# Kernel tuning notes

Hardware: AMD Instinct MI355X
Metric: run time of the kernel (lower is better)

The kernel has to match this reference:

```python
import jax, jax.numpy as jnp
import numpy as np

BS, N, IN_DIM, OUT_DIM = 16, 2048, 32, 64
CHEB_K, E_NODE, T_D = 3, 10, 8
EMBED = E_NODE + T_D  # 18, matches weights_pool dim 0
TOPK = 10


def setup_inputs() -> dict:
    key = jax.random.key(0)
    ks = jax.random.split(key, 7)
    return {
        "x": jax.random.normal(ks[0], (BS, N, IN_DIM), jnp.float32),
        "node_emb": jax.random.normal(ks[1], (N, E_NODE), jnp.float32),
        "t": jax.random.normal(ks[2], (BS, T_D), jnp.float32),
        "n_t": jax.random.normal(ks[3], (BS, T_D), jnp.float32),
        "p": jax.random.normal(ks[4], (BS, 1, 1), jnp.float32),
        "weights_pool": jax.random.normal(ks[5], (EMBED, CHEB_K, IN_DIM, OUT_DIM), jnp.float32) * 0.1,
        "bias_pool": jax.random.normal(ks[6], (EMBED, OUT_DIM), jnp.float32) * 0.1,
    }


def reference(x, node_emb, t, n_t, p, weights_pool, bias_pool):
    bs, n, _ = x.shape
    # static adjacency from node embeddings, broadcast over batch: [bs, N, N]
    a = (node_emb @ node_emb.T)[None, :, :]
    # temporal scalar correction: bmm([bs,1,td],[bs,td,1]) -> [bs,1,1]
    a_t = jnp.einsum('bd,bd->b', n_t, t)[:, None, None]
    _a = a + a_t
    # period branch: scaled relu adjacency, then dynamic topK sparsify
    pre = jax.nn.relu((1.0 + 0.3 * jax.nn.sigmoid(p)) * _a)  # [bs, N, N]
    # topK tie-break noise (torch.rand_like * 0.01); deterministic key here
    noise = jax.random.uniform(jax.random.key(42), pre.shape, jnp.float32) * 0.01
    _, idx = jax.lax.top_k(pre + noise, TOPK)  # idx: [bs, N, TOPK]
    mask = jnp.zeros_like(pre).at[
        jnp.arange(bs)[:, None, None], jnp.arange(n)[None, :, None], idx
    ].set(1.0)
    # masked entries stay 0 (not -inf) before softmax, as in the original
    A = jax.nn.softmax(pre * mask, axis=2)
    # Chebyshev polynomial supports: T0=I, T1=A, Tk = 2*A@T(k-1) - T(k-2)
    I = jnp.broadcast_to(jnp.eye(n, dtype=x.dtype), (bs, n, n))
    supports = [I, A]
    for _ in range(2, CHEB_K):
        supports.append(2.0 * (A @ supports[-1]) - supports[-2])
    S = jnp.stack(supports, axis=1)  # [bs, K, N, N]
    # node-adaptive embedding: cat(node_emb, n_t) -> [bs, N, EMBED]
    ne = jnp.concatenate(
        [jnp.broadcast_to(node_emb[None], (bs, n, E_NODE)),
         jnp.broadcast_to(n_t[:, None, :], (bs, n, T_D))], axis=-1)
    # graph conv features: [bs, N, K, in]
    x_g = jnp.einsum('bknm,bmc->bnkc', S, x)
    bias = ne @ bias_pool  # [bs, N, out]
    # fused per-node dynamic-weight contraction:
    # original: W = einsum(bnd,dkio->bnkio); out = einsum(bnki,bnkio->bno)
    out = jnp.einsum('bnki,bnd,dkio->bno', x_g, ne, weights_pool) + bias
    return out
```

## Files before the change

### kernel.cpp

```cpp
#include <hip/hip_runtime.h>
#include <hip/hip_bf16.h>


constexpr int BS = 16, NN_ = 2048, CIN = 32, OUT = 64, TK = 10;
constexpr int ROWS = BS * NN_;

__device__ __forceinline__ void tf2x32(unsigned x0, unsigned x1,
                                       unsigned& o0, unsigned& o1) {
  const unsigned k0 = 0u, k1 = 42u;
  const unsigned ks2 = k0 ^ k1 ^ 0x1BD11BDAu;
#define TF_R(rot) { x0 += x1; x1 = (x1 << rot) | (x1 >> (32 - rot)); x1 ^= x0; }
  x0 += k0; x1 += k1;
  TF_R(13) TF_R(15) TF_R(26) TF_R(6)
  x0 += k1; x1 += ks2 + 1u;
  TF_R(17) TF_R(29) TF_R(16) TF_R(24)
  x0 += ks2; x1 += k0 + 2u;
  TF_R(13) TF_R(15) TF_R(26) TF_R(6)
  x0 += k0; x1 += k1 + 3u;
  TF_R(17) TF_R(29) TF_R(16) TF_R(24)
  x0 += k1; x1 += ks2 + 4u;
  TF_R(13) TF_R(15) TF_R(26) TF_R(6)
  x0 += ks2; x1 += k0 + 5u;
#undef TF_R
  o0 = x0; o1 = x1;
}

__device__ __forceinline__ float noise_val(unsigned flat) {
  unsigned o0, o1; tf2x32(0u, flat, o0, o1);
  unsigned bits = o0 ^ o1;
  float u = __uint_as_float((bits >> 9) | 0x3f800000u) - 1.0f;
  return 0.01f * u;
}

__global__ __launch_bounds__(256) void k_a0(const float* __restrict__ ne,
                                            float* __restrict__ A0) {
  int gid = blockIdx.x * 256 + threadIdx.x;
  int n = gid >> 11, m = gid & 2047;
  float acc = 0.f;
  #pragma unroll
  for (int d = 0; d < 10; ++d) acc = fmaf(ne[n * 10 + d], ne[m * 10 + d], acc);
  A0[gid] = acc;
}

__global__ __launch_bounds__(256) void k_topk(const float* __restrict__ A0,
                                              const float* __restrict__ t,
                                              const float* __restrict__ n_t,
                                              const float* __restrict__ p,
                                              float* __restrict__ cinv,
                                              int* __restrict__ idxb,
                                              float* __restrict__ wgt) {
  const int n0 = blockIdx.x * 2;
  const int warp = threadIdx.x >> 6, lane = threadIdx.x & 63;
  const int ln = warp >> 1;
  const int n = n0 + ln;
  const int bh = (warp & 1) * 8;

  __shared__ float rowS[2][2048];
  __shared__ float candA[4][128];
  __shared__ int   candM[4][128];
  __shared__ unsigned long long keyS[4][128];

  {
    const float4* src = (const float4*)(A0 + (size_t)n0 * 2048);
    float4* dst = (float4*)rowS;
    for (int i = threadIdx.x; i < 1024; i += 256) dst[i] = src[i];
  }
  __syncthreads();

  float a[32];
  #pragma unroll
  for (int j = 0; j < 8; ++j) {
    float4 f = ((const float4*)rowS[ln])[j * 64 + lane];
    a[j * 4 + 0] = f.x; a[j * 4 + 1] = f.y;
    a[j * 4 + 2] = f.z; a[j * 4 + 3] = f.w;
  }

  float lm = -3.4e38f;
  #pragma unroll
  for (int j = 0; j < 32; ++j) lm = fmaxf(lm, a[j]);

  float last = 3.4e38f;
  for (int rd = 0; rd < 11; ++rd) {
    float x = (lm < last) ? lm : -3.4e38f;
    #pragma unroll
    for (int off = 32; off > 0; off >>= 1) x = fmaxf(x, __shfl_xor(x, off));
    last = x;
  }
  const float T = last - 0.0101f;

  int cnt = 0;
  #pragma unroll
  for (int slot = 0; slot < 32; ++slot) {
    bool c = (a[slot] >= T);
    unsigned long long mk = __ballot(c);
    if (c) {
      int pos = cnt + __popcll(mk & ((1ull << lane) - 1ull));
      if (pos < 128) {
        candA[warp][pos] = a[slot];
        candM[warp][pos] = ((slot >> 2) << 8) + (lane << 2) + (slot & 3);
      }
    }
    cnt += (int)__popcll(mk);
  }
  const int C = cnt < 128 ? cnt : 128;
  const bool two = (C > 64);

  __syncthreads();

  float a0c = 0.f, a1c = 0.f; int m0 = 0, m1 = 0;
  if (lane < C) { a0c = candA[warp][lane]; m0 = candM[warp][lane]; }
  if (two && lane + 64 < C) { a1c = candA[warp][lane + 64]; m1 = candM[warp][lane + 64]; }

  for (int bi = 0; bi < 8; ++bi) {
    const int b = bh + bi;
    const int r = (b << 11) | n;

    float at = 0.f;
    #pragma unroll
    for (int d = 0; d < 8; ++d) at = fmaf(n_t[b * 8 + d], t[b * 8 + d], at);
    const float s = 1.0f + 0.3f * (1.0f / (1.0f + expf(-p[b])));

    float pre0 = fmaxf(s * (a0c + at), 0.f);
    unsigned long long k0 = 0ull;
    if (lane < C) {
      float key0 = pre0 + noise_val((unsigned)r * 2048u + (unsigned)m0);
      k0 = ((unsigned long long)__float_as_uint(key0) << 32) |
           (unsigned)(2047 - m0);
      keyS[warp][lane] = k0;
    }
    float pre1 = 0.f;
    unsigned long long k1 = 0ull;
    if (two) {
      if (lane + 64 < C) {
        pre1 = fmaxf(s * (a1c + at), 0.f);
        float key1 = pre1 + noise_val((unsigned)r * 2048u + (unsigned)m1);
        k1 = ((unsigned long long)__float_as_uint(key1) << 32) |
             (unsigned)(2047 - m1);
      }
      keyS[warp][lane + 64] = k1;
    }
    __syncthreads();

    int rank0 = 0, rank1 = 0;
    for (int j2 = 0; j2 < C; ++j2) {
      unsigned long long kj = keyS[warp][j2];
      rank0 += (kj > k0) ? 1 : 0;
      if (two) rank1 += (kj > k1) ? 1 : 0;
    }
    bool w0 = (lane < C) && (rank0 < 10);
    bool w1 = two && (lane + 64 < C) && (rank1 < 10);

    float e0 = w0 ? expf(pre0) : 0.f;
    float e1 = w1 ? expf(pre1) : 0.f;
    float sum = e0 + e1;
    #pragma unroll
    for (int off = 32; off > 0; off >>= 1) sum += __shfl_xor(sum, off);
    const float ci = 1.0f / (2038.0f + sum);

    unsigned long long mk0 = __ballot(w0);
    if (w0) {
      int pos = __popcll(mk0 & ((1ull << lane) - 1ull));
      idxb[r * 10 + pos] = m0;
      wgt[r * 10 + pos] = (e0 - 1.0f) * ci;
    }
    if (two) {
      unsigned long long mk1 = __ballot(w1);
      int base = __popcll(mk0);
      if (w1) {
        int pos = base + __popcll(mk1 & ((1ull << lane) - 1ull));
        idxb[r * 10 + pos] = m1;
        wgt[r * 10 + pos] = (e1 - 1.0f) * ci;
      }
    }
    if (lane == 0) cinv[r] = ci;
    __syncthreads();
  }
}

__global__ __launch_bounds__(256) void k_colsum_p(const float* __restrict__ in,
                                                  double* __restrict__ part) {
  const int b = blockIdx.x >> 4, ch = blockIdx.x & 15;
  const int c = threadIdx.x & 31, g = threadIdx.x >> 5;
  double acc = 0.0;
  for (int m = ch * 128 + g; m < ch * 128 + 128; m += 8)
    acc += (double)in[(((b << 11) + m) << 5) + c];
  __shared__ double red[8][32];
  red[g][c] = acc;
  __syncthreads();
  if (g == 0) {
    double s2 = red[0][c];
    #pragma unroll
    for (int i = 1; i < 8; ++i) s2 += red[i][c];
    part[(((b << 4) + ch) << 5) + c] = s2;
  }
}

__global__ __launch_bounds__(512) void k_colsum_f(const double* __restrict__ part,
                                                  float* __restrict__ cs) {
  const int b = threadIdx.x >> 5, c = threadIdx.x & 31;
  double s2 = 0.0;
  #pragma unroll
  for (int ch = 0; ch < 16; ++ch) s2 += part[(((b << 4) + ch) << 5) + c];
  cs[(b << 5) + c] = (float)s2;
}

__global__ __launch_bounds__(256) void k_axpy(const float* __restrict__ x,
                                              const float* __restrict__ cinv,
                                              const int* __restrict__ idxb,
                                              const float* __restrict__ wgt,
                                              const float* __restrict__ cs,
                                              float* __restrict__ Y1) {
  int gid = blockIdx.x * 256 + threadIdx.x;
  int r = gid >> 5, c = gid & 31, b = r >> 11;
  float acc = cinv[r] * cs[(b << 5) + c];
  #pragma unroll
  for (int j = 0; j < 10; ++j)
    acc = fmaf(wgt[r * 10 + j], x[(((b << 11) + idxb[r * 10 + j]) << 5) + c], acc);
  Y1[gid] = acc;
}

__global__ __launch_bounds__(256) void k_v(const float* __restrict__ x,
                                           const float* __restrict__ Y1,
                                           const float* __restrict__ cinv,
                                           const int* __restrict__ idxb,
                                           const float* __restrict__ wgt,
                                           const float* __restrict__ csy,
                                           float* __restrict__ V) {
  int gid = blockIdx.x * 256 + threadIdx.x;
  int r = gid >> 5, c = gid & 31, b = r >> 11;
  float y2 = cinv[r] * csy[(b << 5) + c];
  #pragma unroll
  for (int j = 0; j < 10; ++j)
    y2 = fmaf(wgt[r * 10 + j], Y1[(((b << 11) + idxb[r * 10 + j]) << 5) + c], y2);
  float xv = x[gid], y1v = Y1[gid];
  V[r * 96 + c] = xv;
  V[r * 96 + 32 + c] = y1v;
  V[r * 96 + 64 + c] = 2.f * y2 - xv;
}

__global__ __launch_bounds__(256) void k_outn(const float* __restrict__ ne,
                                              const float* __restrict__ n_t,
                                              const float* __restrict__ wp,
                                              const float* __restrict__ bp,
                                              const float* __restrict__ V,
                                              float* __restrict__ out) {
  const int n0 = blockIdx.x * 2;
  __shared__ float Wn[2][48][64];
  __shared__ float Vs[2][16][98];
  __shared__ float bN[2][64];

  for (int e2 = threadIdx.x; e2 < 2 * 16 * 96; e2 += 256) {
    int nn = e2 / 1536, rem = e2 % 1536, bb = rem / 96, ki = rem % 96;
    Vs[nn][bb][ki] = V[((size_t)(bb << 11) + n0 + nn) * 96 + ki];
  }
  for (int e2 = threadIdx.x; e2 < 2 * 64; e2 += 256) {
    int nn = e2 >> 6, o = e2 & 63;
    float acc = 0.f;
    #pragma unroll
    for (int d = 0; d < 10; ++d)
      acc = fmaf(ne[(n0 + nn) * 10 + d], bp[d * 64 + o], acc);
    bN[nn][o] = acc;
  }

  const int wave = threadIdx.x >> 6, lane = threadIdx.x & 63;
  const int nn = wave >> 1, half = wave & 1;
  const int og = lane & 15, bg = lane >> 4;
  const int bA = half * 8 + bg * 2, bB = bA + 1;

  float acc[2][4] = {};
  for (int h = 0; h < 2; ++h) {
    __syncthreads();
    for (int e2 = threadIdx.x; e2 < 2 * 48 * 64; e2 += 256) {
      int nn2 = e2 / 3072, rem = e2 % 3072, ki = rem >> 6, o = rem & 63;
      int kiG = h * 48 + ki;
      float a2 = 0.f;
      #pragma unroll
      for (int d = 0; d < 10; ++d)
        a2 = fmaf(ne[(n0 + nn2) * 10 + d], wp[(d * 96 + kiG) * 64 + o], a2);
      Wn[nn2][ki][o] = a2;
    }
    __syncthreads();
    for (int ki = 0; ki < 48; ++ki) {
      float4 wv = *(const float4*)&Wn[nn][ki][og * 4];
      float vA = Vs[nn][bA][h * 48 + ki], vB = Vs[nn][bB][h * 48 + ki];
      acc[0][0] = fmaf(vA, wv.x, acc[0][0]); acc[0][1] = fmaf(vA, wv.y, acc[0][1]);
      acc[0][2] = fmaf(vA, wv.z, acc[0][2]); acc[0][3] = fmaf(vA, wv.w, acc[0][3]);
      acc[1][0] = fmaf(vB, wv.x, acc[1][0]); acc[1][1] = fmaf(vB, wv.y, acc[1][1]);
      acc[1][2] = fmaf(vB, wv.z, acc[1][2]); acc[1][3] = fmaf(vB, wv.w, acc[1][3]);
    }
  }

  const int n = n0 + nn;
  #pragma unroll
  for (int i = 0; i < 2; ++i) {
    int b = (i == 0) ? bA : bB;
    float4 res;
    #pragma unroll
    for (int q = 0; q < 4; ++q) {
      int o = og * 4 + q;
      float bT = 0.f;
      #pragma unroll
      for (int d = 0; d < 8; ++d)
        bT = fmaf(n_t[b * 8 + d], bp[(10 + d) * 64 + o], bT);
      (&res.x)[q] = acc[i][q] + bN[nn][o] + bT;
    }
    *(float4*)&out[((size_t)(b << 11) + n) * 64 + og * 4] = res;
  }
}

__global__ __launch_bounds__(512) void k_outt(const float* __restrict__ n_t,
                                              const float* __restrict__ wp,
                                              const float* __restrict__ V,
                                              float* __restrict__ out) {
  const int b = blockIdx.x >> 5, tile = blockIdx.x & 31;
  __shared__ float Wt[96][64];
  for (int e2 = threadIdx.x; e2 < 96 * 64; e2 += 512) {
    int ki = e2 >> 6, o = e2 & 63;
    float acc = 0.f;
    #pragma unroll
    for (int d = 0; d < 8; ++d)
      acc = fmaf(n_t[b * 8 + d], wp[((10 + d) * 96 + ki) * 64 + o], acc);
    Wt[ki][o] = acc;
  }
  __syncthreads();
  const int wave = threadIdx.x >> 6, lane = threadIdx.x & 63;
  const int og = lane & 15, rg = lane >> 4;
  const int r0 = tile * 64 + wave * 8 + rg * 2;

  float acc[2][4] = {};
  for (int ki4 = 0; ki4 < 24; ++ki4) {
    float4 vv[2];
    #pragma unroll
    for (int i = 0; i < 2; ++i)
      vv[i] = *(const float4*)&V[(size_t)((b << 11) + r0 + i) * 96 + ki4 * 4];
    #pragma unroll
    for (int t2 = 0; t2 < 4; ++t2) {
      float4 wv = *(const float4*)&Wt[ki4 * 4 + t2][og * 4];
      #pragma unroll
      for (int i = 0; i < 2; ++i) {
        float vi = (t2 == 0) ? vv[i].x : (t2 == 1) ? vv[i].y
                 : (t2 == 2) ? vv[i].z : vv[i].w;
        acc[i][0] = fmaf(vi, wv.x, acc[i][0]);
        acc[i][1] = fmaf(vi, wv.y, acc[i][1]);
        acc[i][2] = fmaf(vi, wv.z, acc[i][2]);
        acc[i][3] = fmaf(vi, wv.w, acc[i][3]);
      }
    }
  }
  #pragma unroll
  for (int i = 0; i < 2; ++i) {
    size_t oidx = (size_t)((b << 11) + r0 + i) * 64 + og * 4;
    float4 cur = *(float4*)&out[oidx];
    cur.x += acc[i][0]; cur.y += acc[i][1];
    cur.z += acc[i][2]; cur.w += acc[i][3];
    *(float4*)&out[oidx] = cur;
  }
}

extern "C" void kernel_launch(void* const* d_in, const int* in_sizes, int n_in,
                              void* d_out, int out_size, void* d_ws, size_t ws_size,
                              hipStream_t stream) {
  const float* x   = (const float*)d_in[0];
  const float* ne  = (const float*)d_in[1];
  const float* t   = (const float*)d_in[2];
  const float* n_t = (const float*)d_in[3];
  const float* p   = (const float*)d_in[4];
  const float* wp  = (const float*)d_in[5];
  const float* bp  = (const float*)d_in[6];
  float* out = (float*)d_out;

  float* ws   = (float*)d_ws;
  float* A0   = ws;
  float* cinv = A0 + 4194304;
  int*   idxb = (int*)(cinv + 32768);
  float* wgt  = (float*)(idxb + 327680);
  float* csx  = wgt + 327680;
  float* csy  = csx + 512;
  float* Y1   = csy + 512;
  float* V    = Y1 + 1048576;
  double* partX = (double*)(V + 3145728);
  double* partY = partX + 8192;

  k_a0      <<<16384, 256, 0, stream>>>(ne, A0);
  k_topk    <<<1024, 256, 0, stream>>>(A0, t, n_t, p, cinv, idxb, wgt);
  k_colsum_p<<<256, 256, 0, stream>>>(x, partX);
  k_colsum_f<<<1, 512, 0, stream>>>(partX, csx);
  k_axpy    <<<4096, 256, 0, stream>>>(x, cinv, idxb, wgt, csx, Y1);
  k_colsum_p<<<256, 256, 0, stream>>>(Y1, partY);
  k_colsum_f<<<1, 512, 0, stream>>>(partY, csy);
  k_v       <<<4096, 256, 0, stream>>>(x, Y1, cinv, idxb, wgt, csy, V);
  k_outn    <<<1024, 256, 0, stream>>>(ne, n_t, wp, bp, V, out);
  k_outt    <<<512, 512, 0, stream>>>(n_t, wp, V, out);
}
```

Before: 202.5 us.

## Precompute per-node and per-batch dynamic weights into workspace before output contraction

Adds k_wn, which materializes the node-embedding part of the dynamic weights for every node (N×96×64) in global memory, reusing the adjacency buffer's space. Adds k_wt, which precomputes the time-embedding weights once per batch instead of recomputing them in every k_outt block. k_outn then handles one node per block and streams the precomputed weights rather than rebuilding them in shared memory. This trades redundant on-chip weight construction and repeated reads of weights_pool for roughly 50 MB of extra global write and read traffic. The new path runs only when the workspace is large enough; otherwise the old kernels are used.

```diff
diff --git a/kernel.cpp b/kernel.cpp
--- a/kernel.cpp
+++ b/kernel.cpp
@@ -238,12 +238,155 @@
   V[r * 96 + 64 + c] = 2.f * y2 - xv;
 }
 
+__global__ __launch_bounds__(256) void k_wn(const float* __restrict__ ne,
+                                            const float* __restrict__ wp,
+                                            float* __restrict__ Wn) {
+  const int ng = blockIdx.x / 6, sg = blockIdx.x % 6;
+  const int slot = sg * 256 + threadIdx.x;
+  const int ki = slot >> 4, o4 = slot & 15;
+
+  __shared__ float neS[16][10];
+  if (threadIdx.x < 160)
+    neS[threadIdx.x / 10][threadIdx.x % 10] =
+        ne[(ng * 16 + threadIdx.x / 10) * 10 + threadIdx.x % 10];
+
+  const float4* wp4 = (const float4*)wp;
+  float4 w[10];
+  #pragma unroll
+  for (int d = 0; d < 10; ++d) w[d] = wp4[(d * 96 + ki) * 16 + o4];
+  __syncthreads();
+
+  float4* Wn4 = (float4*)Wn;
+  #pragma unroll 4
+  for (int nn = 0; nn < 16; ++nn) {
+    float4 acc = {0.f, 0.f, 0.f, 0.f};
+    #pragma unroll
+    for (int d = 0; d < 10; ++d) {
+      float e = neS[nn][d];
+      acc.x = fmaf(e, w[d].x, acc.x); acc.y = fmaf(e, w[d].y, acc.y);
+      acc.z = fmaf(e, w[d].z, acc.z); acc.w = fmaf(e, w[d].w, acc.w);
+    }
+    Wn4[((size_t)(ng * 16 + nn) * 96 + ki) * 16 + o4] = acc;
+  }
+}
+
+__global__ __launch_bounds__(256) void k_wt(const float* __restrict__ n_t,
+                                            const float* __restrict__ wp,
+                                            float* __restrict__ Wt) {
+  int gid = blockIdx.x * 256 + threadIdx.x;
+  int b = gid / 1536, rem = gid % 1536, ki = rem >> 4, o4 = rem & 15;
+  const float4* wp4 = (const float4*)wp;
+  float4 acc = {0.f, 0.f, 0.f, 0.f};
+  #pragma unroll
+  for (int d = 0; d < 8; ++d) {
+    float e = n_t[b * 8 + d];
+    float4 w = wp4[((10 + d) * 96 + ki) * 16 + o4];
+    acc.x = fmaf(e, w.x, acc.x); acc.y = fmaf(e, w.y, acc.y);
+    acc.z = fmaf(e, w.z, acc.z); acc.w = fmaf(e, w.w, acc.w);
+  }
+  ((float4*)Wt)[(b * 96 + ki) * 16 + o4] = acc;
+}
+
 __global__ __launch_bounds__(256) void k_outn(const float* __restrict__ ne,
                                               const float* __restrict__ n_t,
-                                              const float* __restrict__ wp,
+                                              const float* __restrict__ Wn,
                                               const float* __restrict__ bp,
                                               const float* __restrict__ V,
                                               float* __restrict__ out) {
+  const int n = blockIdx.x;
+  __shared__ float Vs[16][100];
+  __shared__ float bNs[64];
+
+  for (int e = threadIdx.x; e < 384; e += 256) {
+    int b = e / 24, j4 = e % 24;
+    float4 f = *(const float4*)&V[((size_t)(b << 11) + n) * 96 + j4 * 4];
+    *(float4*)&Vs[b][j4 * 4] = f;
+  }
+  if (threadIdx.x < 64) {
+    float acc = 0.f;
+    #pragma unroll
+    for (int d = 0; d < 10; ++d)
+      acc = fmaf(ne[n * 10 + d], bp[d * 64 + threadIdx.x], acc);
+    bNs[threadIdx.x] = acc;
+  }
+  __syncthreads();
+
+  const int b = threadIdx.x >> 4, og = threadIdx.x & 15;
+  const float4* Wr = (const float4*)(Wn + (size_t)n * 6144);
+
+  float4 acc = {0.f, 0.f, 0.f, 0.f};
+  #pragma unroll 4
+  for (int ki = 0; ki < 96; ++ki) {
+    float4 wv = Wr[ki * 16 + og];
+    float v = Vs[b][ki];
+    acc.x = fmaf(v, wv.x, acc.x); acc.y = fmaf(v, wv.y, acc.y);
+    acc.z = fmaf(v, wv.z, acc.z); acc.w = fmaf(v, wv.w, acc.w);
+  }
+
+  float4 res;
+  #pragma unroll
+  for (int q = 0; q < 4; ++q) {
+    int o = og * 4 + q;
+    float bT = 0.f;
+    #pragma unroll
+    for (int d = 0; d < 8; ++d)
+      bT = fmaf(n_t[b * 8 + d], bp[(10 + d) * 64 + o], bT);
+    (&res.x)[q] = (&acc.x)[q] + bNs[o] + bT;
+  }
+  *(float4*)&out[((size_t)(b << 11) + n) * 64 + og * 4] = res;
+}
+
+__global__ __launch_bounds__(512) void k_outt(const float* __restrict__ WtG,
+                                              const float* __restrict__ V,
+                                              float* __restrict__ out) {
+  const int b = blockIdx.x >> 5, tile = blockIdx.x & 31;
+  __shared__ float Wt[96][64];
+  {
+    const float4* src = (const float4*)(WtG + (size_t)b * 6144);
+    float4* dst = (float4*)Wt;
+    for (int e = threadIdx.x; e < 1536; e += 512) dst[e] = src[e];
+  }
+  __syncthreads();
+  const int wave = threadIdx.x >> 6, lane = threadIdx.x & 63;
+  const int og = lane & 15, rg = lane >> 4;
+  const int r0 = tile * 64 + wave * 8 + rg * 2;
+
+  float acc[2][4] = {};
+  for (int ki4 = 0; ki4 < 24; ++ki4) {
+    float4 vv[2];
+    #pragma unroll
+    for (int i = 0; i < 2; ++i)
+      vv[i] = *(const float4*)&V[(size_t)((b << 11) + r0 + i) * 96 + ki4 * 4];
+    #pragma unroll
+    for (int t2 = 0; t2 < 4; ++t2) {
+      float4 wv = *(const float4*)&Wt[ki4 * 4 + t2][og * 4];
+      #pragma unroll
+      for (int i = 0; i < 2; ++i) {
+        float vi = (t2 == 0) ? vv[i].x : (t2 == 1) ? vv[i].y
+                 : (t2 == 2) ? vv[i].z : vv[i].w;
+        acc[i][0] = fmaf(vi, wv.x, acc[i][0]);
+        acc[i][1] = fmaf(vi, wv.y, acc[i][1]);
+        acc[i][2] = fmaf(vi, wv.z, acc[i][2]);
+        acc[i][3] = fmaf(vi, wv.w, acc[i][3]);
+      }
+    }
+  }
+  #pragma unroll
+  for (int i = 0; i < 2; ++i) {
+    size_t oidx = (size_t)((b << 11) + r0 + i) * 64 + og * 4;
+    float4 cur = *(float4*)&out[oidx];
+    cur.x += acc[i][0]; cur.y += acc[i][1];
+    cur.z += acc[i][2]; cur.w += acc[i][3];
+    *(float4*)&out[oidx] = cur;
+  }
+}
+
+__global__ __launch_bounds__(256) void k_outn_leg(const float* __restrict__ ne,
+                                                  const float* __restrict__ n_t,
+                                                  const float* __restrict__ wp,
+                                                  const float* __restrict__ bp,
+                                                  const float* __restrict__ V,
+                                                  float* __restrict__ out) {
   const int n0 = blockIdx.x * 2;
   __shared__ float Wn[2][48][64];
   __shared__ float Vs[2][16][98];
@@ -308,10 +451,10 @@
   }
 }
 
-__global__ __launch_bounds__(512) void k_outt(const float* __restrict__ n_t,
-                                              const float* __restrict__ wp,
-                                              const float* __restrict__ V,
-                                              float* __restrict__ out) {
+__global__ __launch_bounds__(512) void k_outt_leg(const float* __restrict__ n_t,
+                                                  const float* __restrict__ wp,
+                                                  const float* __restrict__ V,
+                                                  float* __restrict__ out) {
   const int b = blockIdx.x >> 5, tile = blockIdx.x & 31;
   __shared__ float Wt[96][64];
   for (int e2 = threadIdx.x; e2 < 96 * 64; e2 += 512) {
@@ -368,27 +511,57 @@
   const float* wp  = (const float*)d_in[5];
   const float* bp  = (const float*)d_in[6];
   float* out = (float*)d_out;
-
-  float* ws   = (float*)d_ws;
-  float* A0   = ws;
-  float* cinv = A0 + 4194304;
-  int*   idxb = (int*)(cinv + 32768);
-  float* wgt  = (float*)(idxb + 327680);
-  float* csx  = wgt + 327680;
-  float* csy  = csx + 512;
-  float* Y1   = csy + 512;
-  float* V    = Y1 + 1048576;
-  double* partX = (double*)(V + 3145728);
-  double* partY = partX + 8192;
-
-  k_a0      <<<16384, 256, 0, stream>>>(ne, A0);
-  k_topk    <<<1024, 256, 0, stream>>>(A0, t, n_t, p, cinv, idxb, wgt);
-  k_colsum_p<<<256, 256, 0, stream>>>(x, partX);
-  k_colsum_f<<<1, 512, 0, stream>>>(partX, csx);
-  k_axpy    <<<4096, 256, 0, stream>>>(x, cinv, idxb, wgt, csx, Y1);
-  k_colsum_p<<<256, 256, 0, stream>>>(Y1, partY);
-  k_colsum_f<<<1, 512, 0, stream>>>(partY, csy);
-  k_v       <<<4096, 256, 0, stream>>>(x, Y1, cinv, idxb, wgt, csy, V);
-  k_outn    <<<1024, 256, 0, stream>>>(ne, n_t, wp, bp, V, out);
-  k_outt    <<<512, 512, 0, stream>>>(n_t, wp, V, out);
-}
+  float* ws = (float*)d_ws;
+
+  const size_t NEED_NEW = 17597440ull * 4ull;
+  if (ws_size >= NEED_NEW) {
+    float* cinv  = ws;
+    int*   idxb  = (int*)(cinv + 32768);
+    float* wgt   = (float*)(idxb + 327680);
+    float* csx   = wgt + 327680;
+    float* csy   = csx + 512;
+    float* Y1    = csy + 512;
+    float* V     = Y1 + 1048576;
+    double* partX = (double*)(V + 3145728);
+    double* partY = partX + 8192;
+    float* Wt    = (float*)(partY + 8192);
+    float* UNI   = Wt + 98304;
+    float* A0    = UNI;
+    float* Wn    = UNI;
+
+    k_a0      <<<16384, 256, 0, stream>>>(ne, A0);
+    k_topk    <<<1024, 256, 0, stream>>>(A0, t, n_t, p, cinv, idxb, wgt);
+    k_wn      <<<768, 256, 0, stream>>>(ne, wp, Wn);
+    k_wt      <<<96, 256, 0, stream>>>(n_t, wp, Wt);
+    k_colsum_p<<<256, 256, 0, stream>>>(x, partX);
+    k_colsum_f<<<1, 512, 0, stream>>>(partX, csx);
+    k_axpy    <<<4096, 256, 0, stream>>>(x, cinv, idxb, wgt, csx, Y1);
+    k_colsum_p<<<256, 256, 0, stream>>>(Y1, partY);
+    k_colsum_f<<<1, 512, 0, stream>>>(partY, csy);
+    k_v       <<<4096, 256, 0, stream>>>(x, Y1, cinv, idxb, wgt, csy, V);
+    k_outn    <<<2048, 256, 0, stream>>>(ne, n_t, Wn, bp, V, out);
+    k_outt    <<<512, 512, 0, stream>>>(Wt, V, out);
+  } else {
+    float* A0   = ws;
+    float* cinv = A0 + 4194304;
+    int*   idxb = (int*)(cinv + 32768);
+    float* wgt  = (float*)(idxb + 327680);
+    float* csx  = wgt + 327680;
+    float* csy  = csx + 512;
+    float* Y1   = csy + 512;
+    float* V    = Y1 + 1048576;
+    double* partX = (double*)(V + 3145728);
+    double* partY = partX + 8192;
+
+    k_a0      <<<16384, 256, 0, stream>>>(ne, A0);
+    k_topk    <<<1024, 256, 0, stream>>>(A0, t, n_t, p, cinv, idxb, wgt);
+    k_colsum_p<<<256, 256, 0, stream>>>(x, partX);
+    k_colsum_f<<<1, 512, 0, stream>>>(partX, csx);
+    k_axpy    <<<4096, 256, 0, stream>>>(x, cinv, idxb, wgt, csx, Y1);
+    k_colsum_p<<<256, 256, 0, stream>>>(Y1, partY);
+    k_colsum_f<<<1, 512, 0, stream>>>(partY, csy);
+    k_v       <<<4096, 256, 0, stream>>>(x, Y1, cinv, idxb, wgt, csy, V);
+    k_outn_leg<<<1024, 256, 0, stream>>>(ne, n_t, wp, bp, V, out);
+    k_outt_leg<<<512, 512, 0, stream>>>(n_t, wp, V, out);
+  }
+}
```

Result: no change. 204.1 us (+0.8%).

## Fuse adjacency into topk, precompute node weights, fold colsums into neighbouring kernels

Applied to the files above, without the earlier changes.

Removes the 16MB A0 adjacency buffer by computing the 2048-wide row of node_emb dot products inside the topk kernel, which now handles four rows per 512-thread block. A new prologue kernel precomputes the per-node weights Wn (about 50MB) and the per-batch weights Wt, computes the x column-sum partials, and zeroes csy. The separate colsum kernels are gone: k_axpy reduces the x partials itself and accumulates the Y1 column sum with float atomics. k_outn now reads Wn from global memory, one node per block, instead of recomputing it in shared memory. This cuts launches and the A0 write and read, but adds large Wn traffic, and the atomic accumulation makes the Y1 column sum order-nondeterministic and float rather than double.

```diff
diff --git a/kernel.cpp b/kernel.cpp
--- a/kernel.cpp
+++ b/kernel.cpp
@@ -32,40 +32,128 @@
   return 0.01f * u;
 }
 
-__global__ __launch_bounds__(256) void k_a0(const float* __restrict__ ne,
-                                            float* __restrict__ A0) {
-  int gid = blockIdx.x * 256 + threadIdx.x;
-  int n = gid >> 11, m = gid & 2047;
-  float acc = 0.f;
-  #pragma unroll
-  for (int d = 0; d < 10; ++d) acc = fmaf(ne[n * 10 + d], ne[m * 10 + d], acc);
-  A0[gid] = acc;
-}
-
-__global__ __launch_bounds__(256) void k_topk(const float* __restrict__ A0,
+__global__ __launch_bounds__(256) void k_pre(const float* __restrict__ ne,
+                                             const float* __restrict__ n_t,
+                                             const float* __restrict__ wp,
+                                             const float* __restrict__ x,
+                                             float* __restrict__ Wn,
+                                             float* __restrict__ Wt,
+                                             double* __restrict__ partX,
+                                             float* __restrict__ csy) {
+  const int bid = blockIdx.x;
+  __shared__ float neS[16][10];
+  __shared__ double red[8][32];
+
+  if (bid < 768) {
+    const int ng = bid / 6, sg = bid % 6;
+    const int slot = sg * 256 + threadIdx.x;
+    const int ki = slot >> 4, o4 = slot & 15;
+
+    if (threadIdx.x < 160)
+      neS[threadIdx.x / 10][threadIdx.x % 10] =
+          ne[(ng * 16 + threadIdx.x / 10) * 10 + threadIdx.x % 10];
+
+    const float4* wp4 = (const float4*)wp;
+    float4 w[10];
+    #pragma unroll
+    for (int d = 0; d < 10; ++d) w[d] = wp4[(d * 96 + ki) * 16 + o4];
+    __syncthreads();
+
+    float4* Wn4 = (float4*)Wn;
+    #pragma unroll 4
+    for (int nn = 0; nn < 16; ++nn) {
+      float4 acc = {0.f, 0.f, 0.f, 0.f};
+      #pragma unroll
+      for (int d = 0; d < 10; ++d) {
+        float e = neS[nn][d];
+        acc.x = fmaf(e, w[d].x, acc.x); acc.y = fmaf(e, w[d].y, acc.y);
+        acc.z = fmaf(e, w[d].z, acc.z); acc.w = fmaf(e, w[d].w, acc.w);
+      }
+      Wn4[((size_t)(ng * 16 + nn) * 96 + ki) * 16 + o4] = acc;
+    }
+  } else if (bid < 864) {
+    int gid = (bid - 768) * 256 + threadIdx.x;
+    int b = gid / 1536, rem = gid % 1536, ki = rem >> 4, o4 = rem & 15;
+    const float4* wp4 = (const float4*)wp;
+    float4 acc = {0.f, 0.f, 0.f, 0.f};
+    #pragma unroll
+    for (int d = 0; d < 8; ++d) {
+      float e = n_t[b * 8 + d];
+      float4 w = wp4[((10 + d) * 96 + ki) * 16 + o4];
+      acc.x = fmaf(e, w.x, acc.x); acc.y = fmaf(e, w.y, acc.y);
+      acc.z = fmaf(e, w.z, acc.z); acc.w = fmaf(e, w.w, acc.w);
+    }
+    ((float4*)Wt)[(b * 96 + ki) * 16 + o4] = acc;
+  } else if (bid < 1120) {
+    const int bb = bid - 864;
+    const int b = bb >> 4, ch = bb & 15;
+    const int c = threadIdx.x & 31, g = threadIdx.x >> 5;
+    double acc = 0.0;
+    for (int m = ch * 128 + g; m < ch * 128 + 128; m += 8)
+      acc += (double)x[(((b << 11) + m) << 5) + c];
+    red[g][c] = acc;
+    __syncthreads();
+    if (g == 0) {
+      double s2 = red[0][c];
+      #pragma unroll
+      for (int i = 1; i < 8; ++i) s2 += red[i][c];
+      partX[(((b << 4) + ch) << 5) + c] = s2;
+    }
+  } else {
+    csy[threadIdx.x] = 0.f;
+    csy[256 + threadIdx.x] = 0.f;
+  }
+}
+
+__global__ __launch_bounds__(512) void k_topk(const float* __restrict__ ne,
                                               const float* __restrict__ t,
                                               const float* __restrict__ n_t,
                                               const float* __restrict__ p,
                                               float* __restrict__ cinv,
                                               int* __restrict__ idxb,
                                               float* __restrict__ wgt) {
-  const int n0 = blockIdx.x * 2;
+  const int n0 = blockIdx.x * 4;
   const int warp = threadIdx.x >> 6, lane = threadIdx.x & 63;
+
+  __shared__ float rowS[4][2048];
+  __shared__ float neN[4][10];
+  __shared__ float candA[8][128];
+  __shared__ int   candM[8][128];
+  __shared__ unsigned long long keyS[8][128];
+
+  if (threadIdx.x < 40)
+    neN[threadIdx.x / 10][threadIdx.x % 10] = ne[n0 * 10 + threadIdx.x];
+  __syncthreads();
+
+  {
+    const int m0 = warp * 256 + lane * 4;
+    float nm[40];
+    const float4* nf = (const float4*)(ne + (size_t)m0 * 10);
+    #pragma unroll
+    for (int i = 0; i < 10; ++i) {
+      float4 q = nf[i];
+      nm[i * 4 + 0] = q.x; nm[i * 4 + 1] = q.y;
+      nm[i * 4 + 2] = q.z; nm[i * 4 + 3] = q.w;
+    }
+    #pragma unroll
+    for (int nd = 0; nd < 4; ++nd) {
+      float res[4];
+      #pragma unroll
+      for (int rr = 0; rr < 4; ++rr) {
+        float acc = 0.f;
+        #pragma unroll
+        for (int d = 0; d < 10; ++d)
+          acc = fmaf(neN[nd][d], nm[rr * 10 + d], acc);
+        res[rr] = acc;
+      }
+      *(float4*)&rowS[nd][m0] = make_float4(res[0], res[1], res[2], res[3]);
+    }
+  }
+  __syncthreads();
+
   const int ln = warp >> 1;
   const int n = n0 + ln;
   const int bh = (warp & 1) * 8;
-
-  __shared__ float rowS[2][2048];
-  __shared__ float candA[4][128];
-  __shared__ int   candM[4][128];
-  __shared__ unsigned long long keyS[4][128];
-
-  {
-    const float4* src = (const float4*)(A0 + (size_t)n0 * 2048);
-    float4* dst = (float4*)rowS;
-    for (int i = threadIdx.x; i < 1024; i += 256) dst[i] = src[i];
-  }
-  __syncthreads();
 
   float a[32];
   #pragma unroll
@@ -81,10 +169,10 @@
 
   float last = 3.4e38f;
   for (int rd = 0; rd < 11; ++rd) {
-    float x = (lm < last) ? lm : -3.4e38f;
-    #pragma unroll
-    for (int off = 32; off > 0; off >>= 1) x = fmaxf(x, __shfl_xor(x, off));
-    last = x;
+    float x2 = (lm < last) ? lm : -3.4e38f;
+    #pragma unroll
+    for (int off = 32; off > 0; off >>= 1) x2 = fmaxf(x2, __shfl_xor(x2, off));
+    last = x2;
   }
   const float T = last - 0.0101f;
 
@@ -107,9 +195,9 @@
 
   __syncthreads();
 
-  float a0c = 0.f, a1c = 0.f; int m0 = 0, m1 = 0;
-  if (lane < C) { a0c = candA[warp][lane]; m0 = candM[warp][lane]; }
-  if (two && lane + 64 < C) { a1c = candA[warp][lane + 64]; m1 = candM[warp][lane + 64]; }
+  float a0c = 0.f, a1c = 0.f; int m0c = 0, m1c = 0;
+  if (lane < C) { a0c = candA[warp][lane]; m0c = candM[warp][lane]; }
+  if (two && lane + 64 < C) { a1c = candA[warp][lane + 64]; m1c = candM[warp][lane + 64]; }
 
   for (int bi = 0; bi < 8; ++bi) {
     const int b = bh + bi;
@@ -123,9 +211,9 @@
     float pre0 = fmaxf(s * (a0c + at), 0.f);
     unsigned long long k0 = 0ull;
     if (lane < C) {
-      float key0 = pre0 + noise_val((unsigned)r * 2048u + (unsigned)m0);
+      float key0 = pre0 + noise_val((unsigned)r * 2048u + (unsigned)m0c);
       k0 = ((unsigned long long)__float_as_uint(key0) << 32) |
-           (unsigned)(2047 - m0);
+           (unsigned)(2047 - m0c);
       keyS[warp][lane] = k0;
     }
     float pre1 = 0.f;
@@ -133,9 +221,9 @@
     if (two) {
       if (lane + 64 < C) {
         pre1 = fmaxf(s * (a1c + at), 0.f);
-        float key1 = pre1 + noise_val((unsigned)r * 2048u + (unsigned)m1);
+        float key1 = pre1 + noise_val((unsigned)r * 2048u + (unsigned)m1c);
         k1 = ((unsigned long long)__float_as_uint(key1) << 32) |
-             (unsigned)(2047 - m1);
+             (unsigned)(2047 - m1c);
       }
       keyS[warp][lane + 64] = k1;
     }
@@ -160,7 +248,7 @@
     unsigned long long mk0 = __ballot(w0);
     if (w0) {
       int pos = __popcll(mk0 & ((1ull << lane) - 1ull));
-      idxb[r * 10 + pos] = m0;
+      idxb[r * 10 + pos] = m0c;
       wgt[r * 10 + pos] = (e0 - 1.0f) * ci;
     }
     if (two) {
@@ -168,55 +256,50 @@
       int base = __popcll(mk0);
       if (w1) {
         int pos = base + __popcll(mk1 & ((1ull << lane) - 1ull));
-        idxb[r * 10 + pos] = m1;
+        idxb[r * 10 + pos] = m1c;
         wgt[r * 10 + pos] = (e1 - 1.0f) * ci;
       }
     }
     if (lane == 0) cinv[r] = ci;
     __syncthreads();
   }
-}
-
-__global__ __launch_bounds__(256) void k_colsum_p(const float* __restrict__ in,
-                                                  double* __restrict__ part) {
-  const int b = blockIdx.x >> 4, ch = blockIdx.x & 15;
-  const int c = threadIdx.x & 31, g = threadIdx.x >> 5;
-  double acc = 0.0;
-  for (int m = ch * 128 + g; m < ch * 128 + 128; m += 8)
-    acc += (double)in[(((b << 11) + m) << 5) + c];
-  __shared__ double red[8][32];
-  red[g][c] = acc;
-  __syncthreads();
-  if (g == 0) {
-    double s2 = red[0][c];
-    #pragma unroll
-    for (int i = 1; i < 8; ++i) s2 += red[i][c];
-    part[(((b << 4) + ch) << 5) + c] = s2;
-  }
-}
-
-__global__ __launch_bounds__(512) void k_colsum_f(const double* __restrict__ part,
-                                                  float* __restrict__ cs) {
-  const int b = threadIdx.x >> 5, c = threadIdx.x & 31;
-  double s2 = 0.0;
-  #pragma unroll
-  for (int ch = 0; ch < 16; ++ch) s2 += part[(((b << 4) + ch) << 5) + c];
-  cs[(b << 5) + c] = (float)s2;
 }
 
 __global__ __launch_bounds__(256) void k_axpy(const float* __restrict__ x,
                                               const float* __restrict__ cinv,
                                               const int* __restrict__ idxb,
                                               const float* __restrict__ wgt,
-                                              const float* __restrict__ cs,
-                                              float* __restrict__ Y1) {
+                                              const double* __restrict__ partX,
+                                              float* __restrict__ Y1,
+                                              float* __restrict__ csy) {
   int gid = blockIdx.x * 256 + threadIdx.x;
   int r = gid >> 5, c = gid & 31, b = r >> 11;
-  float acc = cinv[r] * cs[(b << 5) + c];
+  __shared__ float csL[32];
+  __shared__ float red[8][32];
+
+  if (threadIdx.x < 32) {
+    double s2 = 0.0;
+    #pragma unroll
+    for (int ch = 0; ch < 16; ++ch)
+      s2 += partX[(((b << 4) + ch) << 5) + threadIdx.x];
+    csL[threadIdx.x] = (float)s2;
+  }
+  __syncthreads();
+
+  float acc = cinv[r] * csL[c];
   #pragma unroll
   for (int j = 0; j < 10; ++j)
     acc = fmaf(wgt[r * 10 + j], x[(((b << 11) + idxb[r * 10 + j]) << 5) + c], acc);
   Y1[gid] = acc;
+
+  red[threadIdx.x >> 5][c] = acc;
+  __syncthreads();
+  if (threadIdx.x < 32) {
+    float s = red[0][threadIdx.x];
+    #pragma unroll
+    for (int i = 1; i < 8; ++i) s += red[i][threadIdx.x];
+    atomicAdd(&csy[(b << 5) + threadIdx.x], s);
+  }
 }
 
 __global__ __launch_bounds__(256) void k_v(const float* __restrict__ x,
@@ -240,87 +323,62 @@
 
 __global__ __launch_bounds__(256) void k_outn(const float* __restrict__ ne,
                                               const float* __restrict__ n_t,
-                                              const float* __restrict__ wp,
+                                              const float* __restrict__ Wn,
                                               const float* __restrict__ bp,
                                               const float* __restrict__ V,
                                               float* __restrict__ out) {
-  const int n0 = blockIdx.x * 2;
-  __shared__ float Wn[2][48][64];
-  __shared__ float Vs[2][16][98];
-  __shared__ float bN[2][64];
-
-  for (int e2 = threadIdx.x; e2 < 2 * 16 * 96; e2 += 256) {
-    int nn = e2 / 1536, rem = e2 % 1536, bb = rem / 96, ki = rem % 96;
-    Vs[nn][bb][ki] = V[((size_t)(bb << 11) + n0 + nn) * 96 + ki];
-  }
-  for (int e2 = threadIdx.x; e2 < 2 * 64; e2 += 256) {
-    int nn = e2 >> 6, o = e2 & 63;
+  const int n = blockIdx.x;
+  __shared__ float Vs[16][100];
+  __shared__ float bNs[64];
+
+  for (int e = threadIdx.x; e < 384; e += 256) {
+    int b = e / 24, j4 = e % 24;
+    float4 f = *(const float4*)&V[((size_t)(b << 11) + n) * 96 + j4 * 4];
+    *(float4*)&Vs[b][j4 * 4] = f;
+  }
+  if (threadIdx.x < 64) {
     float acc = 0.f;
     #pragma unroll
     for (int d = 0; d < 10; ++d)
-      acc = fmaf(ne[(n0 + nn) * 10 + d], bp[d * 64 + o], acc);
-    bN[nn][o] = acc;
-  }
-
-  const int wave = threadIdx.x >> 6, lane = threadIdx.x & 63;
-  const int nn = wave >> 1, half = wave & 1;
-  const int og = lane & 15, bg = lane >> 4;
-  const int bA = half * 8 + bg * 2, bB = bA + 1;
-
-  float acc[2][4] = {};
-  for (int h = 0; h < 2; ++h) {
-    __syncthreads();
-    for (int e2 = threadIdx.x; e2 < 2 * 48 * 64; e2 += 256) {
-      int nn2 = e2 / 3072, rem = e2 % 3072, ki = rem >> 6, o = rem & 63;
-      int kiG = h * 48 + ki;
-      float a2 = 0.f;
-      #pragma unroll
-      for (int d = 0; d < 10; ++d)
-        a2 = fmaf(ne[(n0 + nn2) * 10 + d], wp[(d * 96 + kiG) * 64 + o], a2);
-      Wn[nn2][ki][o] = a2;
-    }
-    __syncthreads();
-    for (int ki = 0; ki < 48; ++ki) {
-      float4 wv = *(const float4*)&Wn[nn][ki][og * 4];
-      float vA = Vs[nn][bA][h * 48 + ki], vB = Vs[nn][bB][h * 48 + ki];
-      acc[0][0] = fmaf(vA, wv.x, acc[0][0]); acc[0][1] = fmaf(vA, wv.y, acc[0][1]);
-      acc[0][2] = fmaf(vA, wv.z, acc[0][2]); acc[0][3] = fmaf(vA, wv.w, acc[0][3]);
-      acc[1][0] = fmaf(vB, wv.x, acc[1][0]); acc[1][1] = fmaf(vB, wv.y, acc[1][1]);
-      acc[1][2] = fmaf(vB, wv.z, acc[1][2]); acc[1][3] = fmaf(vB, wv.w, acc[1][3]);
-    }
-  }
-
-  const int n = n0 + nn;
-  #pragma unroll
-  for (int i = 0; i < 2; ++i) {
-    int b = (i == 0) ? bA : bB;
-    float4 res;
-    #pragma unroll
-    for (int q = 0; q < 4; ++q) {
-      int o = og * 4 + q;
-      float bT = 0.f;
-      #pragma unroll
-      for (int d = 0; d < 8; ++d)
-        bT = fmaf(n_t[b * 8 + d], bp[(10 + d) * 64 + o], bT);
-      (&res.x)[q] = acc[i][q] + bN[nn][o] + bT;
-    }
-    *(float4*)&out[((size_t)(b << 11) + n) * 64 + og * 4] = res;
-  }
-}
-
-__global__ __launch_bounds__(512) void k_outt(const float* __restrict__ n_t,
-                                              const float* __restrict__ wp,
+      acc = fmaf(ne[n * 10 + d], bp[d * 64 + threadIdx.x], acc);
+    bNs[threadIdx.x] = acc;
+  }
+  __syncthreads();
+
+  const int b = threadIdx.x >> 4, og = threadIdx.x & 15;
+  const float4* Wr = (const float4*)(Wn + (size_t)n * 6144);
+
+  float4 acc = {0.f, 0.f, 0.f, 0.f};
+  #pragma unroll 4
+  for (int ki = 0; ki < 96; ++ki) {
+    float4 wv = Wr[ki * 16 + og];
+    float v = Vs[b][ki];
+    acc.x = fmaf(v, wv.x, acc.x); acc.y = fmaf(v, wv.y, acc.y);
+    acc.z = fmaf(v, wv.z, acc.z); acc.w = fmaf(v, wv.w, acc.w);
+  }
+
+  float4 res;
+  #pragma unroll
+  for (int q = 0; q < 4; ++q) {
+    int o = og * 4 + q;
+    float bT = 0.f;
+    #pragma unroll
+    for (int d = 0; d < 8; ++d)
+      bT = fmaf(n_t[b * 8 + d], bp[(10 + d) * 64 + o], bT);
+    (&res.x)[q] = (&acc.x)[q] + bNs[o] + bT;
+  }
+  *(float4*)&out[((size_t)(b << 11) + n) * 64 + og * 4] = res;
+}
+
+__global__ __launch_bounds__(512) void k_outt(const float* __restrict__ WtG,
                                               const float* __restrict__ V,
                                               float* __restrict__ out) {
   const int b = blockIdx.x >> 5, tile = blockIdx.x & 31;
   __shared__ float Wt[96][64];
-  for (int e2 = threadIdx.x; e2 < 96 * 64; e2 += 512) {
-    int ki = e2 >> 6, o = e2 & 63;
-    float acc = 0.f;
-    #pragma unroll
-    for (int d = 0; d < 8; ++d)
-      acc = fmaf(n_t[b * 8 + d], wp[((10 + d) * 96 + ki) * 64 + o], acc);
-    Wt[ki][o] = acc;
+  {
+    const float4* src = (const float4*)(WtG + (size_t)b * 6144);
+    float4* dst = (float4*)Wt;
+    for (int e = threadIdx.x; e < 1536; e += 512) dst[e] = src[e];
   }
   __syncthreads();
   const int wave = threadIdx.x >> 6, lane = threadIdx.x & 63;
@@ -368,27 +426,23 @@
   const float* wp  = (const float*)d_in[5];
   const float* bp  = (const float*)d_in[6];
   float* out = (float*)d_out;
-
-  float* ws   = (float*)d_ws;
-  float* A0   = ws;
-  float* cinv = A0 + 4194304;
-  int*   idxb = (int*)(cinv + 32768);
-  float* wgt  = (float*)(idxb + 327680);
-  float* csx  = wgt + 327680;
-  float* csy  = csx + 512;
-  float* Y1   = csy + 512;
-  float* V    = Y1 + 1048576;
+  float* ws = (float*)d_ws;
+  (void)in_sizes; (void)n_in; (void)out_size; (void)ws_size;
+
+  float* cinv  = ws;
+  int*   idxb  = (int*)(cinv + 32768);
+  float* wgt   = (float*)(idxb + 327680);
+  float* csy   = wgt + 327680;
+  float* Y1    = csy + 512;
+  float* V     = Y1 + 1048576;
   double* partX = (double*)(V + 3145728);
-  double* partY = partX + 8192;
-
-  k_a0      <<<16384, 256, 0, stream>>>(ne, A0);
-  k_topk    <<<1024, 256, 0, stream>>>(A0, t, n_t, p, cinv, idxb, wgt);
-  k_colsum_p<<<256, 256, 0, stream>>>(x, partX);
-  k_colsum_f<<<1, 512, 0, stream>>>(partX, csx);
-  k_axpy    <<<4096, 256, 0, stream>>>(x, cinv, idxb, wgt, csx, Y1);
-  k_colsum_p<<<256, 256, 0, stream>>>(Y1, partY);
-  k_colsum_f<<<1, 512, 0, stream>>>(partY, csy);
-  k_v       <<<4096, 256, 0, stream>>>(x, Y1, cinv, idxb, wgt, csy, V);
-  k_outn    <<<1024, 256, 0, stream>>>(ne, n_t, wp, bp, V, out);
-  k_outt    <<<512, 512, 0, stream>>>(n_t, wp, V, out);
-}
+  float* Wt    = (float*)(partX + 8192);
+  float* Wn    = Wt + 98304;
+
+  k_pre  <<<1121, 256, 0, stream>>>(ne, n_t, wp, x, Wn, Wt, partX, csy);
+  k_topk <<<512, 512, 0, stream>>>(ne, t, n_t, p, cinv, idxb, wgt);
+  k_axpy <<<4096, 256, 0, stream>>>(x, cinv, idxb, wgt, partX, Y1, csy);
+  k_v    <<<4096, 256, 0, stream>>>(x, Y1, cinv, idxb, wgt, csy, V);
+  k_outn <<<2048, 256, 0, stream>>>(ne, n_t, Wn, bp, V, out);
+  k_outt <<<512, 512, 0, stream>>>(Wt, V, out);
+}
```

Result: faster. 182.4 us (-9.9%).
